# Kernel tuning notes

Measured on AMD Instinct MI355X. Metric: run time of the kernel, lower is better.

## Reference

```python
import jax, jax.numpy as jnp
import numpy as np

N = 100000      # nodes
E = 1600000     # edges (avg degree 16)
D_IN, D_H, D_OUT = 128, 128, 64


def setup_inputs() -> dict:
    key = jax.random.key(0)
    k1, k2, k3, k4 = jax.random.split(key, 4)
    x = jax.random.normal(k1, (N, D_IN), dtype=jnp.float32)
    edge_index = jax.random.randint(k2, (2, E), 0, N, dtype=jnp.int32)
    W1 = jax.random.normal(k3, (D_IN, D_H), dtype=jnp.float32) * (1.0 / np.sqrt(D_IN))
    b1 = jnp.zeros((D_H,), dtype=jnp.float32)
    W2 = jax.random.normal(k4, (D_H, D_OUT), dtype=jnp.float32) * (1.0 / np.sqrt(D_H))
    b2 = jnp.zeros((D_OUT,), dtype=jnp.float32)
    return {"x": x, "edge_index": edge_index, "W1": W1, "b1": b1, "W2": W2, "b2": b2}


def _gcn_conv(x, src, dst, W, b):
    """PyG GCNConv: out = D^{-1/2} (A + I) D^{-1/2} (x W) + b."""
    n = x.shape[0]
    h = x @ W  # [N, D_out] — transform first, then aggregate (PyG order)
    loops = jnp.arange(n, dtype=src.dtype)
    src_f = jnp.concatenate([src, loops])
    dst_f = jnp.concatenate([dst, loops])
    deg = jax.ops.segment_sum(jnp.ones_like(dst_f, dtype=h.dtype), dst_f, num_segments=n)
    dinv = jax.lax.rsqrt(deg)  # deg >= 1 due to self-loops
    norm = dinv[src_f] * dinv[dst_f]            # [E+N]
    msg = h[src_f] * norm[:, None]              # [E+N, D_out] gather
    out = jax.ops.segment_sum(msg, dst_f, num_segments=n)  # scatter-add
    return out + b


def reference(x, edge_index, W1, b1, W2, b2):
    src, dst = edge_index[0], edge_index[1]
    h = jax.nn.relu(_gcn_conv(x, src, dst, W1, b1))
    o = _gcn_conv(h, src, dst, W2, b2)
    return jax.nn.log_softmax(o, axis=1)
```

## Files before the change

kernel.cpp:

```cpp
#include <hip/hip_runtime.h>
#include <hip/hip_bf16.h>

typedef __hip_bfloat16 bf16;
typedef short short8 __attribute__((ext_vector_type(8)));
typedef float f32x4 __attribute__((ext_vector_type(4)));
typedef float f32x2 __attribute__((ext_vector_type(2)));

#define NPB 256
#define MAXBUK 1024

__device__ __forceinline__ float bf2f_raw(unsigned short u) {
    unsigned x = ((unsigned)u) << 16; float f; __builtin_memcpy(&f, &x, 4); return f;
}
__device__ __forceinline__ unsigned short f2bf_raw(float f) {
    unsigned u; __builtin_memcpy(&u, &f, 4);
    u += 0x7FFFu + ((u >> 16) & 1u);
    return (unsigned short)(u >> 16);
}
__device__ __forceinline__ float lo_f(unsigned u) {
    unsigned x = u << 16; float f; __builtin_memcpy(&f, &x, 4); return f;
}
__device__ __forceinline__ float hi_f(unsigned u) {
    unsigned x = u & 0xffff0000u; float f; __builtin_memcpy(&f, &x, 4); return f;
}


__global__ __launch_bounds__(256) void prep_kernel(const unsigned short* __restrict__ W1s,
                                                   const void* __restrict__ W1p,
                                                   const void* __restrict__ W2p,
                                                   const void* __restrict__ b1p,
                                                   const void* __restrict__ b2p,
                                                   unsigned short* __restrict__ WB1,
                                                   unsigned short* __restrict__ WB2,
                                                   float* __restrict__ b1f,
                                                   float* __restrict__ b2f,
                                                   int* __restrict__ flag,
                                                   int* __restrict__ bktcnt,
                                                   int nshorts, int nbuk) {
    __shared__ int red[256];
    const int tt = threadIdx.x;
    const int sample = min(nshorts, 2048);
    int c = 0;
    for (int i = tt; i < sample; i += 256) {
        unsigned e = (W1s[i] >> 7) & 0xFFu;
        if (e >= 140u || (e >= 1u && e <= 40u)) c++;
    }
    red[tt] = c;
    __syncthreads();
    for (int o = 128; o > 0; o >>= 1) {
        if (tt < o) red[tt] += red[tt + o];
        __syncthreads();
    }
    const int isf32 = (red[0] > sample / 8) ? 1 : 0;
    if (blockIdx.x == 0 && tt == 0) *flag = isf32;

    const int t = blockIdx.x * 256 + tt;
    const int T1 = 16384, T2 = 8192;
    if (t < T1) {
        int j = t & 7, l = (t >> 3) & 63, f = t >> 9;
        int n = f >> 2, kk = f & 3;
        int k = kk * 32 + (l >> 4) * 8 + j;
        int col = n * 16 + (l & 15);
        WB1[t] = isf32 ? f2bf_raw(((const float*)W1p)[k * 128 + col])
                       : ((const unsigned short*)W1p)[k * 128 + col];
    } else if (t < T1 + T2) {
        int o = t - T1;
        int j = o & 7, l = (o >> 3) & 63, f = o >> 9;
        int n = f >> 2, kk = f & 3;
        int k = kk * 32 + (l >> 4) * 8 + j;
        int col = n * 16 + (l & 15);
        WB2[o] = isf32 ? f2bf_raw(((const float*)W2p)[k * 64 + col])
                       : ((const unsigned short*)W2p)[k * 64 + col];
    } else if (t < T1 + T2 + 128) {
        int o = t - T1 - T2;
        b1f[o] = isf32 ? ((const float*)b1p)[o] : bf2f_raw(((const unsigned short*)b1p)[o]);
    } else if (t < T1 + T2 + 192) {
        int o = t - T1 - T2 - 128;
        b2f[o] = isf32 ? ((const float*)b2p)[o] : bf2f_raw(((const unsigned short*)b2p)[o]);
    } else if (t < T1 + T2 + 192 + nbuk) {
        bktcnt[t - T1 - T2 - 192] = 0;
    }
}


__global__ __launch_bounds__(256) void ms_count_kernel(const int* __restrict__ dst,
                                                       int* __restrict__ bktcnt,
                                                       int E, int nbuk) {
    __shared__ int cnt[MAXBUK];
    const int t = threadIdx.x;
    const int e0 = blockIdx.x * 4096;
    const int e1 = min(E, e0 + 4096);
    for (int b = t; b < nbuk; b += 256) cnt[b] = 0;
    __syncthreads();
    for (int e = e0 + t; e < e1; e += 256) atomicAdd(&cnt[dst[e] >> 8], 1);
    __syncthreads();
    for (int b = t; b < nbuk; b += 256) {
        int c = cnt[b];
        if (c) atomicAdd(&bktcnt[b], c);
    }
}

__global__ __launch_bounds__(1024) void bscan_kernel(const int* __restrict__ bktcnt,
                                                     int* __restrict__ bofs,
                                                     int* __restrict__ bcur,
                                                     int nbuk, int total) {
    __shared__ int ps[1024];
    const int t = threadIdx.x;
    int v = (t < nbuk) ? bktcnt[t] : 0;
    ps[t] = v;
    __syncthreads();
    for (int o = 1; o < 1024; o <<= 1) {
        int u = (t >= o) ? ps[t - o] : 0;
        __syncthreads();
        ps[t] += u;
        __syncthreads();
    }
    if (t < nbuk) {
        int ex = ps[t] - v;
        bofs[t] = ex;
        bcur[t] = ex;
    }
    if (t == 0) bofs[nbuk] = total;
}

__global__ __launch_bounds__(256) void ms_scatter_kernel(const int* __restrict__ src,
                                                         const int* __restrict__ dst,
                                                         int* __restrict__ bcur,
                                                         unsigned* __restrict__ packed,
                                                         int E, int nbuk) {
    __shared__ int cnt[MAXBUK];
    __shared__ int gbase[MAXBUK];
    const int t = threadIdx.x;
    const int e0 = blockIdx.x * 4096;
    const int e1 = min(E, e0 + 4096);
    for (int b = t; b < nbuk; b += 256) cnt[b] = 0;
    __syncthreads();
    for (int e = e0 + t; e < e1; e += 256) atomicAdd(&cnt[dst[e] >> 8], 1);
    __syncthreads();
    for (int b = t; b < nbuk; b += 256) {
        int c = cnt[b];
        gbase[b] = c ? atomicAdd(&bcur[b], c) : 0;
        cnt[b] = 0;
    }
    __syncthreads();
    for (int e = e0 + t; e < e1; e += 256) {
        int d = dst[e];
        int b = d >> 8;
        int r = atomicAdd(&cnt[b], 1);
        packed[gbase[b] + r] = ((unsigned)(d & 255) << 24) | (unsigned)src[e];
    }
}

__global__ __launch_bounds__(256) void csr_fine2_kernel(const unsigned* __restrict__ packed,
                                                        const int* __restrict__ bofs,
                                                        uint2* __restrict__ nmeta,
                                                        float* __restrict__ dinv,
                                                        unsigned* __restrict__ epu, int n) {
    __shared__ int cnt2[NPB];
    __shared__ int cur[NPB];
    const int t = threadIdx.x;
    const int b = blockIdx.x;
    const int node0 = b << 8;
    const int nn = min(NPB, n - node0);
    cnt2[t] = 0;
    __syncthreads();
    const int beg = bofs[b], end = bofs[b + 1];
    for (int i = beg + t; i < end; i += 256) atomicAdd(&cnt2[packed[i] >> 24], 1);
    __syncthreads();
    int c = cnt2[t];
    cur[t] = c;
    __syncthreads();
    for (int o = 1; o < 256; o <<= 1) {
        int u = (t >= o) ? cur[t - o] : 0;
        __syncthreads();
        cur[t] += u;
        __syncthreads();
    }
    const int base = beg + cur[t] - c;
    if (t < nn) {
        nmeta[node0 + t] = make_uint2((unsigned)base, (unsigned)c);
        dinv[node0 + t] = rsqrtf((float)(c + 1));
    }
    __syncthreads();
    cur[t] = base;
    __syncthreads();
    for (int i = beg + t; i < end; i += 256) {
        unsigned u = packed[i];
        int pos = atomicAdd(&cur[u >> 24], 1);
        epu[2 * pos] = u & 0xFFFFFFu;
    }
}

__global__ __launch_bounds__(256) void epw_kernel(unsigned* __restrict__ epu,
                                                  const float* __restrict__ dinv, int E) {
    int i = blockIdx.x * 256 + threadIdx.x;
    if (i < E) {
        unsigned s = epu[2 * i];
        float w = dinv[s];
        unsigned wb; __builtin_memcpy(&wb, &w, 4);
        epu[2 * i + 1] = wb;
    }
}


__global__ __launch_bounds__(256) void gemm1_mfma(const void* __restrict__ Xp,
                                                  const unsigned short* __restrict__ WB1,
                                                  unsigned short* __restrict__ H, int nrows,
                                                  const int* __restrict__ flag) {
    __shared__ __align__(16) unsigned short Xs[128 * 136];
    __shared__ __align__(16) unsigned short Cs[128 * 68];
    const int t = threadIdx.x;
    const int r0 = blockIdx.x * 128;
    const int isf32 = *flag;

    if (isf32) {
        const float4* Xg = (const float4*)Xp;
        #pragma unroll
        for (int i = 0; i < 16; ++i) {
            int idx = t + 256 * i;
            int row = idx >> 5, c4 = idx & 31;
            float4 v = {0.f, 0.f, 0.f, 0.f};
            if (r0 + row < nrows) v = Xg[(size_t)(r0 + row) * 32 + c4];
            unsigned lo = (unsigned)f2bf_raw(v.x) | ((unsigned)f2bf_raw(v.y) << 16);
            unsigned hi = (unsigned)f2bf_raw(v.z) | ((unsigned)f2bf_raw(v.w) << 16);
            *reinterpret_cast<uint2*>(&Xs[row * 136 + c4 * 4]) = make_uint2(lo, hi);
        }
    } else {
        const uint4* Xg = (const uint4*)Xp;
        #pragma unroll
        for (int i = 0; i < 8; ++i) {
            int idx = t + 256 * i;
            int row = idx >> 4, c8 = idx & 15;
            uint4 v = {0u, 0u, 0u, 0u};
            if (r0 + row < nrows) v = Xg[(size_t)(r0 + row) * 16 + c8];
            *reinterpret_cast<uint4*>(&Xs[row * 136 + c8 * 8]) = v;
        }
    }
    __syncthreads();

    const int lane = t & 63, w = t >> 6;
    const int m0 = w * 32;
    short8 a[2][4];
    #pragma unroll
    for (int rt = 0; rt < 2; ++rt)
        #pragma unroll
        for (int kk = 0; kk < 4; ++kk)
            a[rt][kk] = *reinterpret_cast<const short8*>(
                &Xs[(m0 + rt * 16 + (lane & 15)) * 136 + kk * 32 + (lane >> 4) * 8]);

    for (int p = 0; p < 2; ++p) {
        short8 b[4][4];
        #pragma unroll
        for (int n = 0; n < 4; ++n)
            #pragma unroll
            for (int kk = 0; kk < 4; ++kk)
                b[n][kk] = *reinterpret_cast<const short8*>(
                    WB1 + (size_t)(((p * 4 + n) * 4 + kk) * 64 + lane) * 8);
        f32x4 acc[2][4];
        #pragma unroll
        for (int rt = 0; rt < 2; ++rt)
            #pragma unroll
            for (int n = 0; n < 4; ++n) {
                acc[rt][n] = (f32x4){0.f, 0.f, 0.f, 0.f};
                #pragma unroll
                for (int kk = 0; kk < 4; ++kk)
                    acc[rt][n] = __builtin_amdgcn_mfma_f32_16x16x32_bf16(
                        a[rt][kk], b[n][kk], acc[rt][n], 0, 0, 0);
            }
        if (p) __syncthreads();
        #pragma unroll
        for (int rt = 0; rt < 2; ++rt)
            #pragma unroll
            for (int n = 0; n < 4; ++n)
                #pragma unroll
                for (int r = 0; r < 4; ++r) {
                    int row = m0 + rt * 16 + (lane >> 4) * 4 + r;
                    Cs[row * 68 + n * 16 + (lane & 15)] = f2bf_raw(acc[rt][n][r]);
                }
        __syncthreads();
        #pragma unroll
        for (int i = 0; i < 8; ++i) {
            int idx = t + 256 * i;
            int row = idx >> 4, c4 = idx & 15;
            if (r0 + row < nrows) {
                uint2 v = *reinterpret_cast<const uint2*>(&Cs[row * 68 + c4 * 4]);
                *reinterpret_cast<uint2*>(H + (size_t)(r0 + row) * 128 + p * 64 + c4 * 4) = v;
            }
        }
        if (!p) __syncthreads();
    }
}


__device__ __forceinline__ void acc8v(f32x2* acc, uint4 v, float w) {
    f32x2 wv = {w, w};
    acc[0] += (f32x2){lo_f(v.x), hi_f(v.x)} * wv;
    acc[1] += (f32x2){lo_f(v.y), hi_f(v.y)} * wv;
    acc[2] += (f32x2){lo_f(v.z), hi_f(v.z)} * wv;
    acc[3] += (f32x2){lo_f(v.w), hi_f(v.w)} * wv;
}
__device__ __forceinline__ float epw_f(uint2 e) {
    float w; __builtin_memcpy(&w, &e.y, 4); return w;
}

__global__ __launch_bounds__(128) void agg128_v7(const uint4* __restrict__ H4,
                                                 const uint2* __restrict__ nmeta,
                                                 const uint2* __restrict__ epack,
                                                 const float* __restrict__ biasf,
                                                 uint4* __restrict__ G4, int n) {
    const int lane = threadIdx.x & 63;
    const int g = lane >> 4;
    const int sub = lane & 15;
    const int node = blockIdx.x * 2 + (threadIdx.x >> 6);
    if (node >= n) return;

    const unsigned selfoff = ((unsigned)node << 4) + (unsigned)sub;
    uint4 vself = H4[selfoff];

    const uint2 meta = nmeta[node];
    const int base = (int)meta.x;
    const int cnt = (int)meta.y;
    const int end = base + cnt;
    const float di = rsqrtf((float)(cnt + 1));

    f32x2 acc[4];
    {
        const float ws = (g == 0) ? di : 0.f;
        acc[0] = (f32x2){ws * lo_f(vself.x), ws * hi_f(vself.x)};
        acc[1] = (f32x2){ws * lo_f(vself.y), ws * hi_f(vself.y)};
        acc[2] = (f32x2){ws * lo_f(vself.z), ws * hi_f(vself.z)};
        acc[3] = (f32x2){ws * lo_f(vself.w), ws * hi_f(vself.w)};
    }

    int j = base;
    for (; j + 15 < end; j += 16) {
        uint2 e0 = epack[j + g];
        uint2 e1 = epack[j + 4 + g];
        uint2 e2 = epack[j + 8 + g];
        uint2 e3 = epack[j + 12 + g];
        uint4 v0 = H4[(e0.x << 4) + (unsigned)sub];
        uint4 v1 = H4[(e1.x << 4) + (unsigned)sub];
        uint4 v2 = H4[(e2.x << 4) + (unsigned)sub];
        uint4 v3 = H4[(e3.x << 4) + (unsigned)sub];
        acc8v(acc, v0, epw_f(e0));
        acc8v(acc, v1, epw_f(e1));
        acc8v(acc, v2, epw_f(e2));
        acc8v(acc, v3, epw_f(e3));
    }
    for (; j + 7 < end; j += 8) {
        uint2 e0 = epack[j + g];
        uint2 e1 = epack[j + 4 + g];
        uint4 v0 = H4[(e0.x << 4) + (unsigned)sub];
        uint4 v1 = H4[(e1.x << 4) + (unsigned)sub];
        acc8v(acc, v0, epw_f(e0));
        acc8v(acc, v1, epw_f(e1));
    }
    for (; j + 3 < end; j += 4) {
        uint2 e0 = epack[j + g];
        uint4 v0 = H4[(e0.x << 4) + (unsigned)sub];
        acc8v(acc, v0, epw_f(e0));
    }
    if (j + g < end) {
        uint2 e0 = epack[j + g];
        uint4 v0 = H4[(e0.x << 4) + (unsigned)sub];
        acc8v(acc, v0, epw_f(e0));
    }

    float a8[8];
    #pragma unroll
    for (int i = 0; i < 4; ++i) { a8[2 * i] = acc[i].x; a8[2 * i + 1] = acc[i].y; }
    #pragma unroll
    for (int i = 0; i < 8; ++i) {
        a8[i] += __shfl_xor(a8[i], 16, 64);
        a8[i] += __shfl_xor(a8[i], 32, 64);
    }

    if (g == 0) {
        const float4* b4 = (const float4*)biasf;
        float4 blo = b4[sub * 2], bhi = b4[sub * 2 + 1];
        a8[0] = fmaxf(fmaf(di, a8[0], blo.x), 0.f);
        a8[1] = fmaxf(fmaf(di, a8[1], blo.y), 0.f);
        a8[2] = fmaxf(fmaf(di, a8[2], blo.z), 0.f);
        a8[3] = fmaxf(fmaf(di, a8[3], blo.w), 0.f);
        a8[4] = fmaxf(fmaf(di, a8[4], bhi.x), 0.f);
        a8[5] = fmaxf(fmaf(di, a8[5], bhi.y), 0.f);
        a8[6] = fmaxf(fmaf(di, a8[6], bhi.z), 0.f);
        a8[7] = fmaxf(fmaf(di, a8[7], bhi.w), 0.f);
        uint4 o;
        o.x = (unsigned)f2bf_raw(a8[0]) | ((unsigned)f2bf_raw(a8[1]) << 16);
        o.y = (unsigned)f2bf_raw(a8[2]) | ((unsigned)f2bf_raw(a8[3]) << 16);
        o.z = (unsigned)f2bf_raw(a8[4]) | ((unsigned)f2bf_raw(a8[5]) << 16);
        o.w = (unsigned)f2bf_raw(a8[6]) | ((unsigned)f2bf_raw(a8[7]) << 16);
        G4[selfoff] = o;
    }
}


__global__ __launch_bounds__(256) void gemm2b_mfma(const unsigned short* __restrict__ X,
                                                   const unsigned short* __restrict__ WB2,
                                                   unsigned short* __restrict__ T, int nrows) {
    __shared__ __align__(16) unsigned short Xs[128 * 136];
    __shared__ __align__(16) unsigned short Cs[128 * 68];
    const int t = threadIdx.x;
    const int r0 = blockIdx.x * 128;

    const uint4* Xg = (const uint4*)X;
    #pragma unroll
    for (int i = 0; i < 8; ++i) {
        int idx = t + 256 * i;
        int row = idx >> 4, c8 = idx & 15;
        uint4 v = {0u, 0u, 0u, 0u};
        if (r0 + row < nrows) v = Xg[(size_t)(r0 + row) * 16 + c8];
        *reinterpret_cast<uint4*>(&Xs[row * 136 + c8 * 8]) = v;
    }
    __syncthreads();

    const int lane = t & 63, w = t >> 6;
    const int m0 = w * 32;
    short8 a[2][4];
    #pragma unroll
    for (int rt = 0; rt < 2; ++rt)
        #pragma unroll
        for (int kk = 0; kk < 4; ++kk)
            a[rt][kk] = *reinterpret_cast<const short8*>(
                &Xs[(m0 + rt * 16 + (lane & 15)) * 136 + kk * 32 + (lane >> 4) * 8]);

    short8 b[4][4];
    #pragma unroll
    for (int n = 0; n < 4; ++n)
        #pragma unroll
        for (int kk = 0; kk < 4; ++kk)
            b[n][kk] = *reinterpret_cast<const short8*>(
                WB2 + (size_t)((n * 4 + kk) * 64 + lane) * 8);

    f32x4 acc[2][4];
    #pragma unroll
    for (int rt = 0; rt < 2; ++rt)
        #pragma unroll
        for (int n = 0; n < 4; ++n) {
            acc[rt][n] = (f32x4){0.f, 0.f, 0.f, 0.f};
            #pragma unroll
            for (int kk = 0; kk < 4; ++kk)
                acc[rt][n] = __builtin_amdgcn_mfma_f32_16x16x32_bf16(
                    a[rt][kk], b[n][kk], acc[rt][n], 0, 0, 0);
        }

    __syncthreads();
    #pragma unroll
    for (int rt = 0; rt < 2; ++rt)
        #pragma unroll
        for (int n = 0; n < 4; ++n)
            #pragma unroll
            for (int r = 0; r < 4; ++r) {
                int row = m0 + rt * 16 + (lane >> 4) * 4 + r;
                Cs[row * 68 + n * 16 + (lane & 15)] = f2bf_raw(acc[rt][n][r]);
            }
    __syncthreads();
    #pragma unroll
    for (int i = 0; i < 8; ++i) {
        int idx = t + 256 * i;
        int row = idx >> 4, c4 = idx & 15;
        if (r0 + row < nrows) {
            uint2 v = *reinterpret_cast<const uint2*>(&Cs[row * 68 + c4 * 4]);
            *reinterpret_cast<uint2*>(T + (size_t)(r0 + row) * 64 + c4 * 4) = v;
        }
    }
}


__global__ __launch_bounds__(128) void agg64_final(const uint4* __restrict__ T4,
                                                   const uint2* __restrict__ nmeta,
                                                   const uint2* __restrict__ epack,
                                                   const float* __restrict__ b2f,
                                                   void* __restrict__ OUTv, int n,
                                                   const int* __restrict__ flag) {
    const int lane = threadIdx.x & 63;
    const int g = lane >> 3;
    const int sub = lane & 7;
    const int node = blockIdx.x * 2 + (threadIdx.x >> 6);
    if (node >= n) return;
    const int outf32 = *flag;

    const unsigned selfoff = ((unsigned)node << 3) + (unsigned)sub;
    uint4 vself = T4[selfoff];

    const uint2 meta = nmeta[node];
    const int base = (int)meta.x;
    const int cnt = (int)meta.y;
    const int end = base + cnt;
    const float di = rsqrtf((float)(cnt + 1));

    f32x2 acc[4];
    {
        const float ws = (g == 0) ? di : 0.f;
        acc[0] = (f32x2){ws * lo_f(vself.x), ws * hi_f(vself.x)};
        acc[1] = (f32x2){ws * lo_f(vself.y), ws * hi_f(vself.y)};
        acc[2] = (f32x2){ws * lo_f(vself.z), ws * hi_f(vself.z)};
        acc[3] = (f32x2){ws * lo_f(vself.w), ws * hi_f(vself.w)};
    }

    int j = base;
    for (; j + 15 < end; j += 16) {
        uint2 e0 = epack[j + g];
        uint2 e1 = epack[j + 8 + g];
        uint4 v0 = T4[(e0.x << 3) + (unsigned)sub];
        uint4 v1 = T4[(e1.x << 3) + (unsigned)sub];
        acc8v(acc, v0, epw_f(e0));
        acc8v(acc, v1, epw_f(e1));
    }
    for (; j + 7 < end; j += 8) {
        uint2 e0 = epack[j + g];
        uint4 v0 = T4[(e0.x << 3) + (unsigned)sub];
        acc8v(acc, v0, epw_f(e0));
    }
    if (j + g < end) {
        uint2 e0 = epack[j + g];
        uint4 v0 = T4[(e0.x << 3) + (unsigned)sub];
        acc8v(acc, v0, epw_f(e0));
    }

    float a8[8];
    #pragma unroll
    for (int i = 0; i < 4; ++i) { a8[2 * i] = acc[i].x; a8[2 * i + 1] = acc[i].y; }
    #pragma unroll
    for (int i = 0; i < 8; ++i) {
        a8[i] += __shfl_xor(a8[i], 8, 64);
        a8[i] += __shfl_xor(a8[i], 16, 64);
        a8[i] += __shfl_xor(a8[i], 32, 64);
    }

    if (g == 0) {
        const float4* b4 = (const float4*)b2f;
        float4 blo = b4[sub * 2], bhi = b4[sub * 2 + 1];
        a8[0] = fmaf(di, a8[0], blo.x);
        a8[1] = fmaf(di, a8[1], blo.y);
        a8[2] = fmaf(di, a8[2], blo.z);
        a8[3] = fmaf(di, a8[3], blo.w);
        a8[4] = fmaf(di, a8[4], bhi.x);
        a8[5] = fmaf(di, a8[5], bhi.y);
        a8[6] = fmaf(di, a8[6], bhi.z);
        a8[7] = fmaf(di, a8[7], bhi.w);

        float m = fmaxf(fmaxf(fmaxf(a8[0], a8[1]), fmaxf(a8[2], a8[3])),
                        fmaxf(fmaxf(a8[4], a8[5]), fmaxf(a8[6], a8[7])));
        m = fmaxf(m, __shfl_xor(m, 1, 64));
        m = fmaxf(m, __shfl_xor(m, 2, 64));
        m = fmaxf(m, __shfl_xor(m, 4, 64));
        float s = __expf(a8[0] - m) + __expf(a8[1] - m) + __expf(a8[2] - m) + __expf(a8[3] - m) +
                  __expf(a8[4] - m) + __expf(a8[5] - m) + __expf(a8[6] - m) + __expf(a8[7] - m);
        s += __shfl_xor(s, 1, 64);
        s += __shfl_xor(s, 2, 64);
        s += __shfl_xor(s, 4, 64);
        const float lse = m + __logf(s);

        if (outf32) {
            float4* Of = (float4*)OUTv;
            float4 o0 = {a8[0] - lse, a8[1] - lse, a8[2] - lse, a8[3] - lse};
            float4 o1 = {a8[4] - lse, a8[5] - lse, a8[6] - lse, a8[7] - lse};
            Of[(size_t)node * 16 + sub * 2] = o0;
            Of[(size_t)node * 16 + sub * 2 + 1] = o1;
        } else {
            uint4 o;
            o.x = (unsigned)f2bf_raw(a8[0] - lse) | ((unsigned)f2bf_raw(a8[1] - lse) << 16);
            o.y = (unsigned)f2bf_raw(a8[2] - lse) | ((unsigned)f2bf_raw(a8[3] - lse) << 16);
            o.z = (unsigned)f2bf_raw(a8[4] - lse) | ((unsigned)f2bf_raw(a8[5] - lse) << 16);
            o.w = (unsigned)f2bf_raw(a8[6] - lse) | ((unsigned)f2bf_raw(a8[7] - lse) << 16);
            ((uint4*)OUTv)[(size_t)node * 8 + sub] = o;
        }
    }
}


extern "C" void kernel_launch(void* const* d_in, const int* in_sizes, int n_in,
                              void* d_out, int out_size, void* d_ws, size_t ws_size,
                              hipStream_t stream) {
    const void* x  = d_in[0];
    const int*  ei = (const int*)d_in[1];
    const void* W1 = d_in[2];
    const void* b1 = d_in[3];
    const void* W2 = d_in[4];
    const void* b2 = d_in[5];

    const int N = in_sizes[0] / 128;
    const int E = in_sizes[1] / 2;
    const int* src = ei;
    const int* dst = ei + E;
    const int NBUK = (N + NPB - 1) / NPB;

    char* p = (char*)d_ws;
    auto alloc = [&](size_t bytes) { char* q = p; p += (bytes + 255) & ~255ull; return q; };
    int*   flag   = (int*)  alloc(4);
    uint2* nmeta  = (uint2*)alloc((size_t)N * 8);
    float* dinv   = (float*)alloc((size_t)N * 4);
    int*   bktcnt = (int*)  alloc((size_t)NBUK * 4);
    int*   bofs   = (int*)  alloc((size_t)(NBUK + 1) * 4);
    int*   bcur   = (int*)  alloc((size_t)NBUK * 4);
    float* b1f    = (float*)alloc(128 * 4);
    float* b2f    = (float*)alloc(64 * 4);
    unsigned short* WB1 = (unsigned short*)alloc(16384 * 2);
    unsigned short* WB2 = (unsigned short*)alloc(8192 * 2);
    unsigned* big = (unsigned*)alloc((size_t)N * 128 * 2);
    unsigned* packed = (unsigned*)d_out;
    uint2*    epack  = (uint2*)d_in[1];
    unsigned* g1 = (unsigned*)d_in[0];
    unsigned short* T = (unsigned short*)big;
    (void)ws_size; (void)n_in; (void)out_size;

    const int PREPB = (24768 + NBUK + 255) / 256;
    prep_kernel<<<PREPB, 256, 0, stream>>>((const unsigned short*)W1, W1, W2, b1, b2,
                                           WB1, WB2, b1f, b2f, flag, bktcnt,
                                           in_sizes[2], NBUK);
    const int MSB = (E + 4095) / 4096;
    ms_count_kernel<<<MSB, 256, 0, stream>>>(dst, bktcnt, E, NBUK);
    bscan_kernel<<<1, 1024, 0, stream>>>(bktcnt, bofs, bcur, NBUK, E);
    ms_scatter_kernel<<<MSB, 256, 0, stream>>>(src, dst, bcur, packed, E, NBUK);
    csr_fine2_kernel<<<NBUK, 256, 0, stream>>>(packed, bofs, nmeta, dinv, (unsigned*)epack, N);
    epw_kernel<<<(E + 255) / 256, 256, 0, stream>>>((unsigned*)epack, dinv, E);

    const int GB = (N + 127) / 128;
    gemm1_mfma<<<GB, 256, 0, stream>>>(x, WB1, (unsigned short*)big, N, flag);
    agg128_v7<<<(N + 1) / 2, 128, 0, stream>>>((const uint4*)big, nmeta, epack, b1f, (uint4*)g1, N);
    gemm2b_mfma<<<GB, 256, 0, stream>>>((const unsigned short*)g1, WB2, T, N);
    agg64_final<<<(N + 1) / 2, 128, 0, stream>>>((const uint4*)T, nmeta, epack, b2f, d_out, N, flag);
}
```

Measured before the change: 312.9 us.

## Store layer-1 features in FP8 and fuse preprocessing kernels with graph bucketing

The first GEMM now writes its output as FP8 (e4m3) instead of bf16, and the layer-1 aggregation gathers half as many bytes per neighbour, unpacking with the hardware FP8-to-f32 conversion. Weight prep is fused with bucket counting, and gemm1 is fused with the edge scatter, as block-range branches of two combined kernels. The bucket-count zeroing moves to a memset. The aim is to cut gather bandwidth in the dominant aggregation and to remove launch gaps. The cost is extra quantization error in the hidden features.

```diff
diff --git a/kernel.cpp b/kernel.cpp
--- a/kernel.cpp
+++ b/kernel.cpp
@@ -25,7 +25,7 @@
 }
 
 
-__global__ __launch_bounds__(256) void prep_kernel(const unsigned short* __restrict__ W1s,
+__global__ __launch_bounds__(256) void fatA_kernel(const unsigned short* __restrict__ W1s,
                                                    const void* __restrict__ W1p,
                                                    const void* __restrict__ W2p,
                                                    const void* __restrict__ b1p,
@@ -34,69 +34,63 @@
                                                    unsigned short* __restrict__ WB2,
                                                    float* __restrict__ b1f,
                                                    float* __restrict__ b2f,
-                                                   int* __restrict__ flag,
+                                                   int* __restrict__ flag, int nshorts,
+                                                   const int* __restrict__ dst,
                                                    int* __restrict__ bktcnt,
-                                                   int nshorts, int nbuk) {
-    __shared__ int red[256];
+                                                   int E, int nbuk, int prepb) {
+    __shared__ int smem[MAXBUK];
     const int tt = threadIdx.x;
-    const int sample = min(nshorts, 2048);
-    int c = 0;
-    for (int i = tt; i < sample; i += 256) {
-        unsigned e = (W1s[i] >> 7) & 0xFFu;
-        if (e >= 140u || (e >= 1u && e <= 40u)) c++;
-    }
-    red[tt] = c;
-    __syncthreads();
-    for (int o = 128; o > 0; o >>= 1) {
-        if (tt < o) red[tt] += red[tt + o];
-        __syncthreads();
-    }
-    const int isf32 = (red[0] > sample / 8) ? 1 : 0;
-    if (blockIdx.x == 0 && tt == 0) *flag = isf32;
-
-    const int t = blockIdx.x * 256 + tt;
-    const int T1 = 16384, T2 = 8192;
-    if (t < T1) {
-        int j = t & 7, l = (t >> 3) & 63, f = t >> 9;
-        int n = f >> 2, kk = f & 3;
-        int k = kk * 32 + (l >> 4) * 8 + j;
-        int col = n * 16 + (l & 15);
-        WB1[t] = isf32 ? f2bf_raw(((const float*)W1p)[k * 128 + col])
-                       : ((const unsigned short*)W1p)[k * 128 + col];
-    } else if (t < T1 + T2) {
-        int o = t - T1;
-        int j = o & 7, l = (o >> 3) & 63, f = o >> 9;
-        int n = f >> 2, kk = f & 3;
-        int k = kk * 32 + (l >> 4) * 8 + j;
-        int col = n * 16 + (l & 15);
-        WB2[o] = isf32 ? f2bf_raw(((const float*)W2p)[k * 64 + col])
-                       : ((const unsigned short*)W2p)[k * 64 + col];
-    } else if (t < T1 + T2 + 128) {
-        int o = t - T1 - T2;
-        b1f[o] = isf32 ? ((const float*)b1p)[o] : bf2f_raw(((const unsigned short*)b1p)[o]);
-    } else if (t < T1 + T2 + 192) {
-        int o = t - T1 - T2 - 128;
-        b2f[o] = isf32 ? ((const float*)b2p)[o] : bf2f_raw(((const unsigned short*)b2p)[o]);
-    } else if (t < T1 + T2 + 192 + nbuk) {
-        bktcnt[t - T1 - T2 - 192] = 0;
-    }
-}
-
-
-__global__ __launch_bounds__(256) void ms_count_kernel(const int* __restrict__ dst,
-                                                       int* __restrict__ bktcnt,
-                                                       int E, int nbuk) {
-    __shared__ int cnt[MAXBUK];
-    const int t = threadIdx.x;
-    const int e0 = blockIdx.x * 4096;
-    const int e1 = min(E, e0 + 4096);
-    for (int b = t; b < nbuk; b += 256) cnt[b] = 0;
-    __syncthreads();
-    for (int e = e0 + t; e < e1; e += 256) atomicAdd(&cnt[dst[e] >> 8], 1);
-    __syncthreads();
-    for (int b = t; b < nbuk; b += 256) {
-        int c = cnt[b];
-        if (c) atomicAdd(&bktcnt[b], c);
+    if ((int)blockIdx.x < prepb) {
+        const int sample = min(nshorts, 2048);
+        int c = 0;
+        for (int i = tt; i < sample; i += 256) {
+            unsigned e = (W1s[i] >> 7) & 0xFFu;
+            if (e >= 140u || (e >= 1u && e <= 40u)) c++;
+        }
+        smem[tt] = c;
+        __syncthreads();
+        for (int o = 128; o > 0; o >>= 1) {
+            if (tt < o) smem[tt] += smem[tt + o];
+            __syncthreads();
+        }
+        const int isf32 = (smem[0] > sample / 8) ? 1 : 0;
+        if (blockIdx.x == 0 && tt == 0) *flag = isf32;
+
+        const int t = blockIdx.x * 256 + tt;
+        const int T1 = 16384, T2 = 8192;
+        if (t < T1) {
+            int j = t & 7, l = (t >> 3) & 63, f = t >> 9;
+            int n = f >> 2, kk = f & 3;
+            int k = kk * 32 + (l >> 4) * 8 + j;
+            int col = n * 16 + (l & 15);
+            WB1[t] = isf32 ? f2bf_raw(((const float*)W1p)[k * 128 + col])
+                           : ((const unsigned short*)W1p)[k * 128 + col];
+        } else if (t < T1 + T2) {
+            int o = t - T1;
+            int j = o & 7, l = (o >> 3) & 63, f = o >> 9;
+            int n = f >> 2, kk = f & 3;
+            int k = kk * 32 + (l >> 4) * 8 + j;
+            int col = n * 16 + (l & 15);
+            WB2[o] = isf32 ? f2bf_raw(((const float*)W2p)[k * 64 + col])
+                           : ((const unsigned short*)W2p)[k * 64 + col];
+        } else if (t < T1 + T2 + 128) {
+            int o = t - T1 - T2;
+            b1f[o] = isf32 ? ((const float*)b1p)[o] : bf2f_raw(((const unsigned short*)b1p)[o]);
+        } else if (t < T1 + T2 + 192) {
+            int o = t - T1 - T2 - 128;
+            b2f[o] = isf32 ? ((const float*)b2p)[o] : bf2f_raw(((const unsigned short*)b2p)[o]);
+        }
+    } else {
+        const int e0 = ((int)blockIdx.x - prepb) * 4096;
+        const int e1 = min(E, e0 + 4096);
+        for (int b = tt; b < nbuk; b += 256) smem[b] = 0;
+        __syncthreads();
+        for (int e = e0 + tt; e < e1; e += 256) atomicAdd(&smem[dst[e] >> 8], 1);
+        __syncthreads();
+        for (int b = tt; b < nbuk; b += 256) {
+            int c = smem[b];
+            if (c) atomicAdd(&bktcnt[b], c);
+        }
     }
 }
 
@@ -123,31 +117,127 @@
     if (t == 0) bofs[nbuk] = total;
 }
 
-__global__ __launch_bounds__(256) void ms_scatter_kernel(const int* __restrict__ src,
-                                                         const int* __restrict__ dst,
-                                                         int* __restrict__ bcur,
-                                                         unsigned* __restrict__ packed,
-                                                         int E, int nbuk) {
-    __shared__ int cnt[MAXBUK];
-    __shared__ int gbase[MAXBUK];
+
+__global__ __launch_bounds__(256) void fatB_kernel(const void* __restrict__ Xp,
+                                                   const unsigned short* __restrict__ WB1,
+                                                   unsigned char* __restrict__ Hf8, int nrows,
+                                                   const int* __restrict__ flag,
+                                                   const int* __restrict__ src,
+                                                   const int* __restrict__ dst,
+                                                   int* __restrict__ bcur,
+                                                   unsigned* __restrict__ packed,
+                                                   int E, int nbuk, int gb) {
+    __shared__ __align__(16) char smem[52224];
     const int t = threadIdx.x;
-    const int e0 = blockIdx.x * 4096;
-    const int e1 = min(E, e0 + 4096);
-    for (int b = t; b < nbuk; b += 256) cnt[b] = 0;
-    __syncthreads();
-    for (int e = e0 + t; e < e1; e += 256) atomicAdd(&cnt[dst[e] >> 8], 1);
-    __syncthreads();
-    for (int b = t; b < nbuk; b += 256) {
-        int c = cnt[b];
-        gbase[b] = c ? atomicAdd(&bcur[b], c) : 0;
-        cnt[b] = 0;
-    }
-    __syncthreads();
-    for (int e = e0 + t; e < e1; e += 256) {
-        int d = dst[e];
-        int b = d >> 8;
-        int r = atomicAdd(&cnt[b], 1);
-        packed[gbase[b] + r] = ((unsigned)(d & 255) << 24) | (unsigned)src[e];
+    if ((int)blockIdx.x < gb) {
+        unsigned short* Xs = (unsigned short*)smem;
+        unsigned short* Cs = (unsigned short*)(smem + 34816);
+        const int r0 = blockIdx.x * 128;
+        const int isf32 = *flag;
+
+        if (isf32) {
+            const float4* Xg = (const float4*)Xp;
+            #pragma unroll
+            for (int i = 0; i < 16; ++i) {
+                int idx = t + 256 * i;
+                int row = idx >> 5, c4 = idx & 31;
+                float4 v = {0.f, 0.f, 0.f, 0.f};
+                if (r0 + row < nrows) v = Xg[(size_t)(r0 + row) * 32 + c4];
+                unsigned lo = (unsigned)f2bf_raw(v.x) | ((unsigned)f2bf_raw(v.y) << 16);
+                unsigned hi = (unsigned)f2bf_raw(v.z) | ((unsigned)f2bf_raw(v.w) << 16);
+                *reinterpret_cast<uint2*>(&Xs[row * 136 + c4 * 4]) = make_uint2(lo, hi);
+            }
+        } else {
+            const uint4* Xg = (const uint4*)Xp;
+            #pragma unroll
+            for (int i = 0; i < 8; ++i) {
+                int idx = t + 256 * i;
+                int row = idx >> 4, c8 = idx & 15;
+                uint4 v = {0u, 0u, 0u, 0u};
+                if (r0 + row < nrows) v = Xg[(size_t)(r0 + row) * 16 + c8];
+                *reinterpret_cast<uint4*>(&Xs[row * 136 + c8 * 8]) = v;
+            }
+        }
+        __syncthreads();
+
+        const int lane = t & 63, w = t >> 6;
+        const int m0 = w * 32;
+        short8 a[2][4];
+        #pragma unroll
+        for (int rt = 0; rt < 2; ++rt)
+            #pragma unroll
+            for (int kk = 0; kk < 4; ++kk)
+                a[rt][kk] = *reinterpret_cast<const short8*>(
+                    &Xs[(m0 + rt * 16 + (lane & 15)) * 136 + kk * 32 + (lane >> 4) * 8]);
+
+        for (int p = 0; p < 2; ++p) {
+            short8 b[4][4];
+            #pragma unroll
+            for (int n = 0; n < 4; ++n)
+                #pragma unroll
+                for (int kk = 0; kk < 4; ++kk)
+                    b[n][kk] = *reinterpret_cast<const short8*>(
+                        WB1 + (size_t)(((p * 4 + n) * 4 + kk) * 64 + lane) * 8);
+            f32x4 acc[2][4];
+            #pragma unroll
+            for (int rt = 0; rt < 2; ++rt)
+                #pragma unroll
+                for (int n = 0; n < 4; ++n) {
+                    acc[rt][n] = (f32x4){0.f, 0.f, 0.f, 0.f};
+                    #pragma unroll
+                    for (int kk = 0; kk < 4; ++kk)
+                        acc[rt][n] = __builtin_amdgcn_mfma_f32_16x16x32_bf16(
+                            a[rt][kk], b[n][kk], acc[rt][n], 0, 0, 0);
+                }
+            if (p) __syncthreads();
+            #pragma unroll
+            for (int rt = 0; rt < 2; ++rt)
+                #pragma unroll
+                for (int n = 0; n < 4; ++n)
+                    #pragma unroll
+                    for (int r = 0; r < 4; ++r) {
+                        int row = m0 + rt * 16 + (lane >> 4) * 4 + r;
+                        Cs[row * 68 + n * 16 + (lane & 15)] = f2bf_raw(acc[rt][n][r]);
+                    }
+            __syncthreads();
+            #pragma unroll
+            for (int i = 0; i < 4; ++i) {
+                int idx = t + 256 * i;
+                int row = idx >> 3, c8 = idx & 7;
+                if (r0 + row < nrows) {
+                    uint2 va = *reinterpret_cast<const uint2*>(&Cs[row * 68 + c8 * 8]);
+                    uint2 vb = *reinterpret_cast<const uint2*>(&Cs[row * 68 + c8 * 8 + 4]);
+                    int w0 = __builtin_amdgcn_cvt_pk_fp8_f32(lo_f(va.x), hi_f(va.x), 0, false);
+                    w0 = __builtin_amdgcn_cvt_pk_fp8_f32(lo_f(va.y), hi_f(va.y), w0, true);
+                    int w1 = __builtin_amdgcn_cvt_pk_fp8_f32(lo_f(vb.x), hi_f(vb.x), 0, false);
+                    w1 = __builtin_amdgcn_cvt_pk_fp8_f32(lo_f(vb.y), hi_f(vb.y), w1, true);
+                    *reinterpret_cast<uint2*>(Hf8 + (size_t)(r0 + row) * 128 + p * 64 + c8 * 8) =
+                        make_uint2((unsigned)w0, (unsigned)w1);
+                }
+            }
+            if (!p) __syncthreads();
+        }
+    } else {
+        int* cnt = (int*)smem;
+        int* gbase = (int*)(smem + 4096);
+        const int e0 = ((int)blockIdx.x - gb) * 4096;
+        const int e1 = min(E, e0 + 4096);
+        for (int b = t; b < nbuk; b += 256) cnt[b] = 0;
+        __syncthreads();
+        for (int e = e0 + t; e < e1; e += 256) atomicAdd(&cnt[dst[e] >> 8], 1);
+        __syncthreads();
+        for (int b = t; b < nbuk; b += 256) {
+            int c = cnt[b];
+            gbase[b] = c ? atomicAdd(&bcur[b], c) : 0;
+            cnt[b] = 0;
+        }
+        __syncthreads();
+        for (int e = e0 + t; e < e1; e += 256) {
+            int d = dst[e];
+            int b = d >> 8;
+            int r = atomicAdd(&cnt[b], 1);
+            packed[gbase[b] + r] = ((unsigned)(d & 255) << 24) | (unsigned)src[e];
+        }
     }
 }
 
@@ -203,107 +293,19 @@
 }
 
 
-__global__ __launch_bounds__(256) void gemm1_mfma(const void* __restrict__ Xp,
-                                                  const unsigned short* __restrict__ WB1,
-                                                  unsigned short* __restrict__ H, int nrows,
-                                                  const int* __restrict__ flag) {
-    __shared__ __align__(16) unsigned short Xs[128 * 136];
-    __shared__ __align__(16) unsigned short Cs[128 * 68];
-    const int t = threadIdx.x;
-    const int r0 = blockIdx.x * 128;
-    const int isf32 = *flag;
-
-    if (isf32) {
-        const float4* Xg = (const float4*)Xp;
-        #pragma unroll
-        for (int i = 0; i < 16; ++i) {
-            int idx = t + 256 * i;
-            int row = idx >> 5, c4 = idx & 31;
-            float4 v = {0.f, 0.f, 0.f, 0.f};
-            if (r0 + row < nrows) v = Xg[(size_t)(r0 + row) * 32 + c4];
-            unsigned lo = (unsigned)f2bf_raw(v.x) | ((unsigned)f2bf_raw(v.y) << 16);
-            unsigned hi = (unsigned)f2bf_raw(v.z) | ((unsigned)f2bf_raw(v.w) << 16);
-            *reinterpret_cast<uint2*>(&Xs[row * 136 + c4 * 4]) = make_uint2(lo, hi);
-        }
-    } else {
-        const uint4* Xg = (const uint4*)Xp;
-        #pragma unroll
-        for (int i = 0; i < 8; ++i) {
-            int idx = t + 256 * i;
-            int row = idx >> 4, c8 = idx & 15;
-            uint4 v = {0u, 0u, 0u, 0u};
-            if (r0 + row < nrows) v = Xg[(size_t)(r0 + row) * 16 + c8];
-            *reinterpret_cast<uint4*>(&Xs[row * 136 + c8 * 8]) = v;
-        }
-    }
-    __syncthreads();
-
-    const int lane = t & 63, w = t >> 6;
-    const int m0 = w * 32;
-    short8 a[2][4];
-    #pragma unroll
-    for (int rt = 0; rt < 2; ++rt)
-        #pragma unroll
-        for (int kk = 0; kk < 4; ++kk)
-            a[rt][kk] = *reinterpret_cast<const short8*>(
-                &Xs[(m0 + rt * 16 + (lane & 15)) * 136 + kk * 32 + (lane >> 4) * 8]);
-
-    for (int p = 0; p < 2; ++p) {
-        short8 b[4][4];
-        #pragma unroll
-        for (int n = 0; n < 4; ++n)
-            #pragma unroll
-            for (int kk = 0; kk < 4; ++kk)
-                b[n][kk] = *reinterpret_cast<const short8*>(
-                    WB1 + (size_t)(((p * 4 + n) * 4 + kk) * 64 + lane) * 8);
-        f32x4 acc[2][4];
-        #pragma unroll
-        for (int rt = 0; rt < 2; ++rt)
-            #pragma unroll
-            for (int n = 0; n < 4; ++n) {
-                acc[rt][n] = (f32x4){0.f, 0.f, 0.f, 0.f};
-                #pragma unroll
-                for (int kk = 0; kk < 4; ++kk)
-                    acc[rt][n] = __builtin_amdgcn_mfma_f32_16x16x32_bf16(
-                        a[rt][kk], b[n][kk], acc[rt][n], 0, 0, 0);
-            }
-        if (p) __syncthreads();
-        #pragma unroll
-        for (int rt = 0; rt < 2; ++rt)
-            #pragma unroll
-            for (int n = 0; n < 4; ++n)
-                #pragma unroll
-                for (int r = 0; r < 4; ++r) {
-                    int row = m0 + rt * 16 + (lane >> 4) * 4 + r;
-                    Cs[row * 68 + n * 16 + (lane & 15)] = f2bf_raw(acc[rt][n][r]);
-                }
-        __syncthreads();
-        #pragma unroll
-        for (int i = 0; i < 8; ++i) {
-            int idx = t + 256 * i;
-            int row = idx >> 4, c4 = idx & 15;
-            if (r0 + row < nrows) {
-                uint2 v = *reinterpret_cast<const uint2*>(&Cs[row * 68 + c4 * 4]);
-                *reinterpret_cast<uint2*>(H + (size_t)(r0 + row) * 128 + p * 64 + c4 * 4) = v;
-            }
-        }
-        if (!p) __syncthreads();
-    }
-}
-
-
-__device__ __forceinline__ void acc8v(f32x2* acc, uint4 v, float w) {
-    f32x2 wv = {w, w};
-    acc[0] += (f32x2){lo_f(v.x), hi_f(v.x)} * wv;
-    acc[1] += (f32x2){lo_f(v.y), hi_f(v.y)} * wv;
-    acc[2] += (f32x2){lo_f(v.z), hi_f(v.z)} * wv;
-    acc[3] += (f32x2){lo_f(v.w), hi_f(v.w)} * wv;
-}
 __device__ __forceinline__ float epw_f(uint2 e) {
     float w; __builtin_memcpy(&w, &e.y, 4); return w;
 }
 
-__global__ __launch_bounds__(128) void agg128_v7(const uint4* __restrict__ H4,
+__device__ __forceinline__ void accf8_2(f32x2* acc, uint2 v, float w) {
+    f32x2 wv = {w, w};
+    acc[0] += __builtin_amdgcn_cvt_pk_f32_fp8(v.x, false) * wv;
+    acc[1] += __builtin_amdgcn_cvt_pk_f32_fp8(v.x, true)  * wv;
+    acc[2] += __builtin_amdgcn_cvt_pk_f32_fp8(v.y, false) * wv;
+    acc[3] += __builtin_amdgcn_cvt_pk_f32_fp8(v.y, true)  * wv;
+}
+
+__global__ __launch_bounds__(128) void agg128_v9(const uint2* __restrict__ H2,
                                                  const uint2* __restrict__ nmeta,
                                                  const uint2* __restrict__ epack,
                                                  const float* __restrict__ biasf,
@@ -314,8 +316,7 @@
     const int node = blockIdx.x * 2 + (threadIdx.x >> 6);
     if (node >= n) return;
 
-    const unsigned selfoff = ((unsigned)node << 4) + (unsigned)sub;
-    uint4 vself = H4[selfoff];
+    uint2 vself = H2[((unsigned)node << 4) + (unsigned)sub];
 
     const uint2 meta = nmeta[node];
     const int base = (int)meta.x;
@@ -324,13 +325,9 @@
     const float di = rsqrtf((float)(cnt + 1));
 
     f32x2 acc[4];
-    {
-        const float ws = (g == 0) ? di : 0.f;
-        acc[0] = (f32x2){ws * lo_f(vself.x), ws * hi_f(vself.x)};
-        acc[1] = (f32x2){ws * lo_f(vself.y), ws * hi_f(vself.y)};
-        acc[2] = (f32x2){ws * lo_f(vself.z), ws * hi_f(vself.z)};
-        acc[3] = (f32x2){ws * lo_f(vself.w), ws * hi_f(vself.w)};
-    }
+    #pragma unroll
+    for (int i = 0; i < 4; ++i) acc[i] = (f32x2){0.f, 0.f};
+    accf8_2(acc, vself, (g == 0) ? di : 0.f);
 
     int j = base;
     for (; j + 15 < end; j += 16) {
@@ -338,32 +335,32 @@
         uint2 e1 = epack[j + 4 + g];
         uint2 e2 = epack[j + 8 + g];
         uint2 e3 = epack[j + 12 + g];
-        uint4 v0 = H4[(e0.x << 4) + (unsigned)sub];
-        uint4 v1 = H4[(e1.x << 4) + (unsigned)sub];
-        uint4 v2 = H4[(e2.x << 4) + (unsigned)sub];
-        uint4 v3 = H4[(e3.x << 4) + (unsigned)sub];
-        acc8v(acc, v0, epw_f(e0));
-        acc8v(acc, v1, epw_f(e1));
-        acc8v(acc, v2, epw_f(e2));
-        acc8v(acc, v3, epw_f(e3));
+        uint2 v0 = H2[(e0.x << 4) + (unsigned)sub];
+        uint2 v1 = H2[(e1.x << 4) + (unsigned)sub];
+        uint2 v2 = H2[(e2.x << 4) + (unsigned)sub];
+        uint2 v3 = H2[(e3.x << 4) + (unsigned)sub];
+        accf8_2(acc, v0, epw_f(e0));
+        accf8_2(acc, v1, epw_f(e1));
+        accf8_2(acc, v2, epw_f(e2));
+        accf8_2(acc, v3, epw_f(e3));
     }
     for (; j + 7 < end; j += 8) {
         uint2 e0 = epack[j + g];
         uint2 e1 = epack[j + 4 + g];
-        uint4 v0 = H4[(e0.x << 4) + (unsigned)sub];
-        uint4 v1 = H4[(e1.x << 4) + (unsigned)sub];
-        acc8v(acc, v0, epw_f(e0));
-        acc8v(acc, v1, epw_f(e1));
+        uint2 v0 = H2[(e0.x << 4) + (unsigned)sub];
+        uint2 v1 = H2[(e1.x << 4) + (unsigned)sub];
+        accf8_2(acc, v0, epw_f(e0));
+        accf8_2(acc, v1, epw_f(e1));
     }
     for (; j + 3 < end; j += 4) {
         uint2 e0 = epack[j + g];
-        uint4 v0 = H4[(e0.x << 4) + (unsigned)sub];
-        acc8v(acc, v0, epw_f(e0));
+        uint2 v0 = H2[(e0.x << 4) + (unsigned)sub];
+        accf8_2(acc, v0, epw_f(e0));
     }
     if (j + g < end) {
         uint2 e0 = epack[j + g];
-        uint4 v0 = H4[(e0.x << 4) + (unsigned)sub];
-        acc8v(acc, v0, epw_f(e0));
+        uint2 v0 = H2[(e0.x << 4) + (unsigned)sub];
+        accf8_2(acc, v0, epw_f(e0));
     }
 
     float a8[8];
@@ -391,7 +388,7 @@
         o.y = (unsigned)f2bf_raw(a8[2]) | ((unsigned)f2bf_raw(a8[3]) << 16);
         o.z = (unsigned)f2bf_raw(a8[4]) | ((unsigned)f2bf_raw(a8[5]) << 16);
         o.w = (unsigned)f2bf_raw(a8[6]) | ((unsigned)f2bf_raw(a8[7]) << 16);
-        G4[selfoff] = o;
+        G4[((unsigned)node << 4) + (unsigned)sub] = o;
     }
 }
 
@@ -467,6 +464,14 @@
     }
 }
 
+
+__device__ __forceinline__ void acc8v(f32x2* acc, uint4 v, float w) {
+    f32x2 wv = {w, w};
+    acc[0] += (f32x2){lo_f(v.x), hi_f(v.x)} * wv;
+    acc[1] += (f32x2){lo_f(v.y), hi_f(v.y)} * wv;
+    acc[2] += (f32x2){lo_f(v.z), hi_f(v.z)} * wv;
+    acc[3] += (f32x2){lo_f(v.w), hi_f(v.w)} * wv;
+}
 
 __global__ __launch_bounds__(128) void agg64_final(const uint4* __restrict__ T4,
                                                    const uint2* __restrict__ nmeta,
@@ -606,20 +611,21 @@
     unsigned short* T = (unsigned short*)big;
     (void)ws_size; (void)n_in; (void)out_size;
 
-    const int PREPB = (24768 + NBUK + 255) / 256;
-    prep_kernel<<<PREPB, 256, 0, stream>>>((const unsigned short*)W1, W1, W2, b1, b2,
-                                           WB1, WB2, b1f, b2f, flag, bktcnt,
-                                           in_sizes[2], NBUK);
+    const int PREPB = 97;
     const int MSB = (E + 4095) / 4096;
-    ms_count_kernel<<<MSB, 256, 0, stream>>>(dst, bktcnt, E, NBUK);
+    const int GB = (N + 127) / 128;
+
+    hipMemsetAsync(bktcnt, 0, (size_t)NBUK * 4, stream);
+    fatA_kernel<<<PREPB + MSB, 256, 0, stream>>>((const unsigned short*)W1, W1, W2, b1, b2,
+                                                 WB1, WB2, b1f, b2f, flag, in_sizes[2],
+                                                 dst, bktcnt, E, NBUK, PREPB);
     bscan_kernel<<<1, 1024, 0, stream>>>(bktcnt, bofs, bcur, NBUK, E);
-    ms_scatter_kernel<<<MSB, 256, 0, stream>>>(src, dst, bcur, packed, E, NBUK);
+    fatB_kernel<<<GB + MSB, 256, 0, stream>>>(x, WB1, (unsigned char*)big, N, flag,
+                                              src, dst, bcur, packed, E, NBUK, GB);
     csr_fine2_kernel<<<NBUK, 256, 0, stream>>>(packed, bofs, nmeta, dinv, (unsigned*)epack, N);
     epw_kernel<<<(E + 255) / 256, 256, 0, stream>>>((unsigned*)epack, dinv, E);
 
-    const int GB = (N + 127) / 128;
-    gemm1_mfma<<<GB, 256, 0, stream>>>(x, WB1, (unsigned short*)big, N, flag);
-    agg128_v7<<<(N + 1) / 2, 128, 0, stream>>>((const uint4*)big, nmeta, epack, b1f, (uint4*)g1, N);
+    agg128_v9<<<(N + 1) / 2, 128, 0, stream>>>((const uint2*)big, nmeta, epack, b1f, (uint4*)g1, N);
     gemm2b_mfma<<<GB, 256, 0, stream>>>((const unsigned short*)g1, WB2, T, N);
     agg64_final<<<(N + 1) / 2, 128, 0, stream>>>((const uint4*)T, nmeta, epack, b2f, d_out, N, flag);
 }
```

New measurement: 299.3 us. 1.05x faster.
